# Kernel tuning notes

Hardware: AMD Instinct MI355X
Metric: run time of the kernel (lower is better)

The kernel has to match this reference:

```python
import jax, jax.numpy as jnp
import numpy as np


def setup_inputs() -> dict:
    key = jax.random.key(0)
    ks = jax.random.split(key, 10)
    B, N, F, H = 4, 512, 64, 4
    x = jax.random.normal(ks[0], (B, N, F), dtype=jnp.float32)
    adj = jax.random.uniform(ks[1], (N, N), dtype=jnp.float32)
    s = 1.0 / np.sqrt(F)
    Wq = jax.random.normal(ks[2], (F, F * H), dtype=jnp.float32) * s
    bq = jnp.zeros((F * H,), dtype=jnp.float32)
    Wk = jax.random.normal(ks[3], (F, F * H), dtype=jnp.float32) * s
    bk = jnp.zeros((F * H,), dtype=jnp.float32)
    Wlin = jax.random.normal(ks[4], (H, F), dtype=jnp.float32) * (1.0 / np.sqrt(H))
    blin = jnp.zeros((F,), dtype=jnp.float32)
    Wfc = jax.random.normal(ks[5], (F, F), dtype=jnp.float32) * s
    bfc = jnp.zeros((F,), dtype=jnp.float32)
    return {"x": x, "adj": adj, "Wq": Wq, "bq": bq, "Wk": Wk, "bk": bk,
            "Wlin": Wlin, "blin": blin, "Wfc": Wfc, "bfc": bfc}


def reference(x, adj, Wq, bq, Wk, bk, Wlin, blin, Wfc, bfc):
    B, N, F = x.shape
    H = Wlin.shape[0]
    # multi-head attention matrix (value projection is computed but unused in the original)
    q = (x @ Wq + bq).reshape(B, N, H, F)  # [B,N,H,F]
    k = (x @ Wk + bk).reshape(B, N, H, F)
    scores = jnp.einsum('bihf,bjhf->bhij', q, k) / jnp.sqrt(jnp.float32(F))
    attn = jax.nn.softmax(scores, axis=-1)  # [B,H,N,N]
    # linear over heads: [B,N,N,H] @ [H,F] -> [B,N,N,F]
    SV2 = jnp.einsum('bhij,hf->bijf', attn, Wlin) + blin
    # symmetric normalization of (adj + I)
    A = adj + jnp.eye(N, dtype=adj.dtype)
    d = jnp.sum(A, axis=1) ** -0.5
    noradj = d[:, None] * A * d[None, :]  # [N,N]
    # sum over dim 1 (source index i) of noradj[i,j]*SV2[b,i,j,f]*x[b,j,f]
    S = jnp.einsum('ij,bijf->bjf', noradj, SV2)
    sx = x * S  # [B,N,F]
    out = jnp.einsum('ij,bjf->bif', noradj, sx)
    out = out @ Wfc + bfc
    return jax.nn.relu(out)
```

## Files before the change

### kernel.cpp

```cpp
#include <hip/hip_runtime.h>
#include <math.h>

#define NN 512
#define FF 64
#define HH 4


__global__ __launch_bounds__(512) void k_s1(const float* __restrict__ x,
                                            const float* __restrict__ Wq,
                                            const float* __restrict__ bq,
                                            const float* __restrict__ Wk,
                                            const float* __restrict__ bk,
                                            const float* __restrict__ adj,
                                            float* __restrict__ q_t,
                                            float* __restrict__ kT,
                                            float* __restrict__ dinv,
                                            float* __restrict__ T,
                                            float* __restrict__ cvec) {
    __shared__ float x_lds[4][64];
    int blk = blockIdx.x, tid = threadIdx.x;
    int wave = tid >> 6, lane = tid & 63;
    int b = blk >> 7, itile = blk & 127;
    int i0 = itile * 4;

    if (wave >= 4) {
        int idx = tid - 256;
        x_lds[idx >> 6][idx & 63] = x[((long)b * NN + i0 + (idx >> 6)) * FF + (idx & 63)];
    } else if (wave == 0) {
        float acc = 0.f;
#pragma unroll
        for (int k = 0; k < 8; ++k) acc += adj[blk * NN + k * 64 + lane];
        for (int o = 32; o > 0; o >>= 1) acc += __shfl_xor(acc, o);
        if (lane == 0) dinv[blk] = 1.0f / sqrtf(acc + 1.0f);
    } else if (wave == 1) {
        if (lane < 16) T[blk * 16 + lane] = 0.f;
    } else if (wave == 2) {
        if (lane == 0) cvec[blk] = 0.f;
    }
    __syncthreads();

    int isK = tid >> 8, col = tid & 255;
    const float* W = isK ? Wk : Wq;
    float bv = (isK ? bk : bq)[col];
    float a0 = bv, a1 = bv, a2 = bv, a3 = bv;
#pragma unroll 8
    for (int cc = 0; cc < 64; ++cc) {
        float w = W[cc * 256 + col];
        a0 = fmaf(x_lds[0][cc], w, a0);
        a1 = fmaf(x_lds[1][cc], w, a1);
        a2 = fmaf(x_lds[2][cc], w, a2);
        a3 = fmaf(x_lds[3][cc], w, a3);
    }
    int h = col >> 6, f = col & 63;
    int bh = b * HH + h;
    if (!isK) {
        long base = ((long)bh * NN + i0) * FF + f;
        q_t[base] = a0; q_t[base + FF] = a1;
        q_t[base + 2 * FF] = a2; q_t[base + 3 * FF] = a3;
    } else {
        long base = ((long)bh * FF + f) * NN + i0;
        *(float4*)(kT + base) = make_float4(a0, a1, a2, a3);
    }
}

__global__ __launch_bounds__(512) void k_s2(const float* __restrict__ q_t,
                                            const float* __restrict__ kT,
                                            const float* __restrict__ adj,
                                            const float* __restrict__ dinv,
                                            float* __restrict__ T,
                                            float* __restrict__ cvec) {
    __shared__ float q_lds[8][64];
    __shared__ float red[8][8];
    __shared__ float red2[8][8];
    int blk = blockIdx.x, tid = threadIdx.x;
    int itile = blk & 63, h = (blk >> 6) & 3, b = blk >> 8;
    int bh = b * HH + h, i0 = itile * 8;
    int wv = tid >> 6, lane = tid & 63;

    q_lds[tid >> 6][tid & 63] = q_t[((long)bh * NN + i0 + (tid >> 6)) * FF + (tid & 63)];
    __syncthreads();

    int j = tid;
    const float* kb = kT + (long)bh * FF * NN;
    float s[8];
#pragma unroll
    for (int r = 0; r < 8; ++r) s[r] = 0.f;
#pragma unroll 2
    for (int f4 = 0; f4 < 64; f4 += 4) {
        float kv[4];
#pragma unroll
        for (int u = 0; u < 4; ++u) kv[u] = kb[(f4 + u) * NN + j];
#pragma unroll
        for (int r = 0; r < 8; ++r) {
            float4 qv = *(const float4*)&q_lds[r][f4];
            s[r] = fmaf(qv.x, kv[0], s[r]);
            s[r] = fmaf(qv.y, kv[1], s[r]);
            s[r] = fmaf(qv.z, kv[2], s[r]);
            s[r] = fmaf(qv.w, kv[3], s[r]);
        }
    }
    const float scale = 0.125f;
#pragma unroll
    for (int r = 0; r < 8; ++r) {
        float v = s[r];
        for (int o = 32; o > 0; o >>= 1) v = fmaxf(v, __shfl_xor(v, o));
        if (lane == 0) red[r][wv] = v;
    }
    __syncthreads();
    float m[8];
#pragma unroll
    for (int r = 0; r < 8; ++r) {
        float v = red[r][0];
#pragma unroll
        for (int w = 1; w < 8; ++w) v = fmaxf(v, red[r][w]);
        m[r] = v;
    }
#pragma unroll
    for (int r = 0; r < 8; ++r) {
        s[r] = expf((s[r] - m[r]) * scale);
        float v = s[r];
        for (int o = 32; o > 0; o >>= 1) v += __shfl_xor(v, o);
        if (lane == 0) red2[r][wv] = v;
    }
    __syncthreads();
    float Zi[8];
#pragma unroll
    for (int r = 0; r < 8; ++r) {
        float v = red2[r][0];
#pragma unroll
        for (int w = 1; w < 8; ++w) v += red2[r][w];
        Zi[r] = 1.0f / v;
    }
    float dj = dinv[j];
    float pw = 0.f, cw = 0.f;
#pragma unroll
    for (int r = 0; r < 8; ++r) {
        int gi = i0 + r;
        float di = dinv[gi];
        float a = adj[(long)gi * NN + j] + (gi == j ? 1.f : 0.f);
        float t = di * a;
        pw = fmaf(t, s[r] * Zi[r], pw);
        cw += t;
    }
    atomicAdd(&T[bh * NN + j], pw * dj);
    if (b == 0 && h == 0) atomicAdd(&cvec[j], cw);
}

__global__ __launch_bounds__(256) void k_s3(const float* __restrict__ x,
                                            const float* __restrict__ T,
                                            const float* __restrict__ Wlin,
                                            const float* __restrict__ blin,
                                            const float* __restrict__ cvec,
                                            const float* __restrict__ adj,
                                            const float* __restrict__ dinv,
                                            const float* __restrict__ Wfc,
                                            const float* __restrict__ bfc,
                                            float* __restrict__ out) {
    __shared__ float4 u4_l[NN];
    __shared__ float  u0_l[NN];
    __shared__ float2 ad_l[NN];
    __shared__ float part[4][2][64];
    __shared__ float m_lds[2][64];
    __shared__ float part2[4][2][64];
    int blk = blockIdx.x, tid = threadIdx.x;
    int b = blk >> 8, itile = blk & 255;
    int i0 = itile * 2;

    for (int jj = tid; jj < NN; jj += 256) {
        float dj = dinv[jj];
        u0_l[jj] = dj * dj * cvec[jj];
        u4_l[jj] = make_float4(dj * T[(b * HH + 0) * NN + jj],
                               dj * T[(b * HH + 1) * NN + jj],
                               dj * T[(b * HH + 2) * NN + jj],
                               dj * T[(b * HH + 3) * NN + jj]);
        ad_l[jj] = make_float2(adj[(long)i0 * NN + jj] + (i0 == jj ? 1.f : 0.f),
                               adj[(long)(i0 + 1) * NN + jj] + (i0 + 1 == jj ? 1.f : 0.f));
    }
    __syncthreads();

    int f = tid & 63, jc = tid >> 6;
    int jb = jc * 128;
    float blf = blin[f];
    float4 wl = make_float4(Wlin[f], Wlin[64 + f], Wlin[128 + f], Wlin[192 + f]);
    const float* xb = x + (long)b * NN * FF + f;
    float a0 = 0.f, a1 = 0.f;
#pragma unroll 4
    for (int j = jb; j < jb + 128; ++j) {
        float xv = xb[(long)j * FF];
        float4 u = u4_l[j];
        float2 ad = ad_l[j];
        float S = blf * u0_l[j];
        S = fmaf(wl.x, u.x, S);
        S = fmaf(wl.y, u.y, S);
        S = fmaf(wl.z, u.z, S);
        S = fmaf(wl.w, u.w, S);
        float sx = xv * S;
        a0 = fmaf(ad.x, sx, a0);
        a1 = fmaf(ad.y, sx, a1);
    }
    part[jc][0][f] = a0;
    part[jc][1][f] = a1;
    __syncthreads();
    if (jc == 0) {
        m_lds[0][f] = (part[0][0][f] + part[1][0][f] + part[2][0][f] + part[3][0][f]) * dinv[i0];
        m_lds[1][f] = (part[0][1][f] + part[1][1][f] + part[2][1][f] + part[3][1][f]) * dinv[i0 + 1];
    }
    __syncthreads();
    float o0 = 0.f, o1 = 0.f;
    int c0 = jc * 16;
#pragma unroll
    for (int cc = 0; cc < 16; ++cc) {
        float w = Wfc[(c0 + cc) * FF + f];
        o0 = fmaf(m_lds[0][c0 + cc], w, o0);
        o1 = fmaf(m_lds[1][c0 + cc], w, o1);
    }
    part2[jc][0][f] = o0;
    part2[jc][1][f] = o1;
    __syncthreads();
    if (jc == 0) {
        float bb = bfc[f];
        float r0 = part2[0][0][f] + part2[1][0][f] + part2[2][0][f] + part2[3][0][f] + bb;
        float r1 = part2[0][1][f] + part2[1][1][f] + part2[2][1][f] + part2[3][1][f] + bb;
        out[((long)b * NN + i0) * FF + f]     = fmaxf(r0, 0.f);
        out[((long)b * NN + i0 + 1) * FF + f] = fmaxf(r1, 0.f);
    }
}

extern "C" void kernel_launch(void* const* d_in, const int* in_sizes, int n_in,
                              void* d_out, int out_size, void* d_ws, size_t ws_size,
                              hipStream_t stream) {
    const float* x    = (const float*)d_in[0];
    const float* adj  = (const float*)d_in[1];
    const float* Wq   = (const float*)d_in[2];
    const float* bq   = (const float*)d_in[3];
    const float* Wk   = (const float*)d_in[4];
    const float* bk   = (const float*)d_in[5];
    const float* Wlin = (const float*)d_in[6];
    const float* blin = (const float*)d_in[7];
    const float* Wfc  = (const float*)d_in[8];
    const float* bfc  = (const float*)d_in[9];
    float* out = (float*)d_out;

    float* ws   = (float*)d_ws;
    float* dinv = ws;
    float* cvec = ws + 512;
    float* T    = ws + 1024;
    float* q_t  = ws + 9216;
    float* kT   = ws + 2106368;

    k_s1<<<dim3(512), dim3(512), 0, stream>>>(x, Wq, bq, Wk, bk, adj, q_t, kT, dinv, T, cvec);
    k_s2<<<dim3(1024), dim3(512), 0, stream>>>(q_t, kT, adj, dinv, T, cvec);
    k_s3<<<dim3(1024), dim3(256), 0, stream>>>(x, T, Wlin, blin, cvec, adj, dinv, Wfc, bfc, out);
}
```

Measured before the change: 117.2 us.

## Tile QK^T in LDS with register blocking and row-major K layout

The score kernel now handles 16 query rows per block and stages K in swizzled LDS tiles. Each thread computes a 2x8 register tile from float4 LDS reads, replacing the earlier per-column global reads of a transposed K. The projection kernel is split into separate Q and K blocks of 256 threads and writes K row-major. Partial sums are reduced with shuffles before the atomics, which cuts the atomic count. This aims to raise arithmetic reuse and coalescing in the attention stage, at the cost of more LDS traffic, extra barriers and higher register use.

```diff
diff --git a/kernel.cpp b/kernel.cpp
--- a/kernel.cpp
+++ b/kernel.cpp
@@ -6,144 +6,221 @@
 #define HH 4
 
 
-__global__ __launch_bounds__(512) void k_s1(const float* __restrict__ x,
+__global__ __launch_bounds__(256) void k_s1(const float* __restrict__ x,
                                             const float* __restrict__ Wq,
                                             const float* __restrict__ bq,
                                             const float* __restrict__ Wk,
                                             const float* __restrict__ bk,
                                             const float* __restrict__ adj,
                                             float* __restrict__ q_t,
-                                            float* __restrict__ kT,
+                                            float* __restrict__ k_t,
                                             float* __restrict__ dinv,
                                             float* __restrict__ T,
                                             float* __restrict__ cvec) {
     __shared__ float x_lds[4][64];
     int blk = blockIdx.x, tid = threadIdx.x;
     int wave = tid >> 6, lane = tid & 63;
-    int b = blk >> 7, itile = blk & 127;
-    int i0 = itile * 4;
-
-    if (wave >= 4) {
-        int idx = tid - 256;
-        x_lds[idx >> 6][idx & 63] = x[((long)b * NN + i0 + (idx >> 6)) * FF + (idx & 63)];
-    } else if (wave == 0) {
+
+    if (blk < 512 && wave == 0) {
         float acc = 0.f;
 #pragma unroll
-        for (int k = 0; k < 8; ++k) acc += adj[blk * NN + k * 64 + lane];
+        for (int k = 0; k < 8; ++k) acc += adj[(long)blk * NN + k * 64 + lane];
         for (int o = 32; o > 0; o >>= 1) acc += __shfl_xor(acc, o);
         if (lane == 0) dinv[blk] = 1.0f / sqrtf(acc + 1.0f);
-    } else if (wave == 1) {
-        if (lane < 16) T[blk * 16 + lane] = 0.f;
-    } else if (wave == 2) {
-        if (lane == 0) cvec[blk] = 0.f;
-    }
-    __syncthreads();
-
-    int isK = tid >> 8, col = tid & 255;
+    }
+    if (blk < 128 && wave == 1) T[blk * 64 + lane] = 0.f;
+    if (blk < 8 && wave == 2) cvec[blk * 64 + lane] = 0.f;
+
+    int b = blk >> 8, rest = blk & 255, isK = rest >> 7, itile = rest & 127;
+    int i0 = itile * 4;
+    x_lds[tid >> 6][tid & 63] = x[((long)b * NN + i0 + (tid >> 6)) * FF + (tid & 63)];
+    __syncthreads();
     const float* W = isK ? Wk : Wq;
-    float bv = (isK ? bk : bq)[col];
+    float bv = (isK ? bk : bq)[tid];
     float a0 = bv, a1 = bv, a2 = bv, a3 = bv;
-#pragma unroll 8
     for (int cc = 0; cc < 64; ++cc) {
-        float w = W[cc * 256 + col];
+        float w = W[cc * 256 + tid];
         a0 = fmaf(x_lds[0][cc], w, a0);
         a1 = fmaf(x_lds[1][cc], w, a1);
         a2 = fmaf(x_lds[2][cc], w, a2);
         a3 = fmaf(x_lds[3][cc], w, a3);
     }
-    int h = col >> 6, f = col & 63;
-    int bh = b * HH + h;
-    if (!isK) {
-        long base = ((long)bh * NN + i0) * FF + f;
-        q_t[base] = a0; q_t[base + FF] = a1;
-        q_t[base + 2 * FF] = a2; q_t[base + 3 * FF] = a3;
-    } else {
-        long base = ((long)bh * FF + f) * NN + i0;
-        *(float4*)(kT + base) = make_float4(a0, a1, a2, a3);
-    }
+    int h = tid >> 6, f = tid & 63;
+    float* dst = (isK ? k_t : q_t) + ((long)(b * HH + h) * NN + i0) * FF + f;
+    dst[0] = a0; dst[FF] = a1; dst[2 * FF] = a2; dst[3 * FF] = a3;
 }
 
 __global__ __launch_bounds__(512) void k_s2(const float* __restrict__ q_t,
-                                            const float* __restrict__ kT,
+                                            const float* __restrict__ k_t,
                                             const float* __restrict__ adj,
                                             const float* __restrict__ dinv,
                                             float* __restrict__ T,
                                             float* __restrict__ cvec) {
-    __shared__ float q_lds[8][64];
-    __shared__ float red[8][8];
-    __shared__ float red2[8][8];
+    __shared__ float ql[16 * 68];
+    __shared__ float kl[512 * 16];
+    __shared__ float redm[8][16];
+    __shared__ float redz[8][16];
     int blk = blockIdx.x, tid = threadIdx.x;
-    int itile = blk & 63, h = (blk >> 6) & 3, b = blk >> 8;
-    int bh = b * HH + h, i0 = itile * 8;
-    int wv = tid >> 6, lane = tid & 63;
-
-    q_lds[tid >> 6][tid & 63] = q_t[((long)bh * NN + i0 + (tid >> 6)) * FF + (tid & 63)];
-    __syncthreads();
-
-    int j = tid;
-    const float* kb = kT + (long)bh * FF * NN;
-    float s[8];
-#pragma unroll
-    for (int r = 0; r < 8; ++r) s[r] = 0.f;
-#pragma unroll 2
-    for (int f4 = 0; f4 < 64; f4 += 4) {
-        float kv[4];
-#pragma unroll
-        for (int u = 0; u < 4; ++u) kv[u] = kb[(f4 + u) * NN + j];
-#pragma unroll
-        for (int r = 0; r < 8; ++r) {
-            float4 qv = *(const float4*)&q_lds[r][f4];
-            s[r] = fmaf(qv.x, kv[0], s[r]);
-            s[r] = fmaf(qv.y, kv[1], s[r]);
-            s[r] = fmaf(qv.z, kv[2], s[r]);
-            s[r] = fmaf(qv.w, kv[3], s[r]);
-        }
-    }
+    int bh = blk >> 5, itile = blk & 31;
+    int i0 = itile * 16;
+    int wv = tid >> 6;
+    int ig = tid & 7, jg = tid >> 3;
+
+    if (tid < 256) {
+        int r = tid >> 4, c4 = tid & 15;
+        *(float4*)&ql[r * 68 + c4 * 4] =
+            *(const float4*)(q_t + ((long)bh * NN + i0 + r) * FF + c4 * 4);
+    }
+
+    float acc[2][8];
+#pragma unroll
+    for (int ii = 0; ii < 2; ++ii)
+#pragma unroll
+        for (int jj = 0; jj < 8; ++jj) acc[ii][jj] = 0.f;
+
+    const float* kb = k_t + (long)bh * NN * FF;
+#pragma unroll
+    for (int cc = 0; cc < 4; ++cc) {
+#pragma unroll
+        for (int w = 0; w < 4; ++w) {
+            int v = w * 512 + tid;
+            int row = v >> 2, c4 = v & 3;
+            int slot = c4 ^ ((row >> 3) & 3);
+            *(float4*)&kl[row * 16 + slot * 4] =
+                *(const float4*)(kb + (long)row * FF + cc * 16 + c4 * 4);
+        }
+        __syncthreads();
+#pragma unroll
+        for (int k4 = 0; k4 < 4; ++k4) {
+            float4 qf[2], kf[8];
+#pragma unroll
+            for (int ii = 0; ii < 2; ++ii)
+                qf[ii] = *(const float4*)&ql[(ig * 2 + ii) * 68 + cc * 16 + k4 * 4];
+#pragma unroll
+            for (int jj = 0; jj < 8; ++jj) {
+                int j = jg * 8 + jj;
+                int slot = k4 ^ ((j >> 3) & 3);
+                kf[jj] = *(const float4*)&kl[j * 16 + slot * 4];
+            }
+#pragma unroll
+            for (int ii = 0; ii < 2; ++ii)
+#pragma unroll
+                for (int jj = 0; jj < 8; ++jj) {
+                    acc[ii][jj] = fmaf(qf[ii].x, kf[jj].x, acc[ii][jj]);
+                    acc[ii][jj] = fmaf(qf[ii].y, kf[jj].y, acc[ii][jj]);
+                    acc[ii][jj] = fmaf(qf[ii].z, kf[jj].z, acc[ii][jj]);
+                    acc[ii][jj] = fmaf(qf[ii].w, kf[jj].w, acc[ii][jj]);
+                }
+        }
+        __syncthreads();
+    }
+
+#pragma unroll
+    for (int w = 0; w < 4; ++w) {
+        int v = w * 512 + tid;
+        int r = v >> 7, c4 = v & 127;
+        *(float4*)&kl[r * 512 + c4 * 4] =
+            *(const float4*)(adj + (long)(i0 + r) * NN + c4 * 4);
+    }
+
     const float scale = 0.125f;
-#pragma unroll
-    for (int r = 0; r < 8; ++r) {
-        float v = s[r];
-        for (int o = 32; o > 0; o >>= 1) v = fmaxf(v, __shfl_xor(v, o));
-        if (lane == 0) red[r][wv] = v;
-    }
-    __syncthreads();
-    float m[8];
-#pragma unroll
-    for (int r = 0; r < 8; ++r) {
-        float v = red[r][0];
-#pragma unroll
-        for (int w = 1; w < 8; ++w) v = fmaxf(v, red[r][w]);
-        m[r] = v;
-    }
-#pragma unroll
-    for (int r = 0; r < 8; ++r) {
-        s[r] = expf((s[r] - m[r]) * scale);
-        float v = s[r];
-        for (int o = 32; o > 0; o >>= 1) v += __shfl_xor(v, o);
-        if (lane == 0) red2[r][wv] = v;
-    }
-    __syncthreads();
-    float Zi[8];
-#pragma unroll
-    for (int r = 0; r < 8; ++r) {
-        float v = red2[r][0];
-#pragma unroll
-        for (int w = 1; w < 8; ++w) v += red2[r][w];
-        Zi[r] = 1.0f / v;
-    }
-    float dj = dinv[j];
-    float pw = 0.f, cw = 0.f;
-#pragma unroll
-    for (int r = 0; r < 8; ++r) {
-        int gi = i0 + r;
-        float di = dinv[gi];
-        float a = adj[(long)gi * NN + j] + (gi == j ? 1.f : 0.f);
-        float t = di * a;
-        pw = fmaf(t, s[r] * Zi[r], pw);
-        cw += t;
-    }
-    atomicAdd(&T[bh * NN + j], pw * dj);
-    if (b == 0 && h == 0) atomicAdd(&cvec[j], cw);
+    float m[2], Zi[2];
+#pragma unroll
+    for (int ii = 0; ii < 2; ++ii) {
+        float v = acc[ii][0];
+#pragma unroll
+        for (int jj = 1; jj < 8; ++jj) v = fmaxf(v, acc[ii][jj]);
+        v = fmaxf(v, __shfl_xor(v, 8));
+        v = fmaxf(v, __shfl_xor(v, 16));
+        v = fmaxf(v, __shfl_xor(v, 32));
+        if ((tid & 63) < 8) redm[wv][ig * 2 + ii] = v;
+    }
+    __syncthreads();
+#pragma unroll
+    for (int ii = 0; ii < 2; ++ii) {
+        int row = ig * 2 + ii;
+        float v = redm[0][row];
+#pragma unroll
+        for (int w = 1; w < 8; ++w) v = fmaxf(v, redm[w][row]);
+        m[ii] = v;
+    }
+#pragma unroll
+    for (int ii = 0; ii < 2; ++ii) {
+        float z = 0.f;
+#pragma unroll
+        for (int jj = 0; jj < 8; ++jj) {
+            float p = expf((acc[ii][jj] - m[ii]) * scale);
+            acc[ii][jj] = p;
+            z += p;
+        }
+        z += __shfl_xor(z, 8);
+        z += __shfl_xor(z, 16);
+        z += __shfl_xor(z, 32);
+        if ((tid & 63) < 8) redz[wv][ig * 2 + ii] = z;
+    }
+    __syncthreads();
+#pragma unroll
+    for (int ii = 0; ii < 2; ++ii) {
+        int row = ig * 2 + ii;
+        float z = redz[0][row];
+#pragma unroll
+        for (int w = 1; w < 8; ++w) z += redz[w][row];
+        Zi[ii] = 1.0f / z;
+    }
+
+    float di[2];
+    di[0] = dinv[i0 + ig * 2];
+    di[1] = dinv[i0 + ig * 2 + 1];
+    float cs[8], cw[8];
+#pragma unroll
+    for (int jj = 0; jj < 8; ++jj) { cs[jj] = 0.f; cw[jj] = 0.f; }
+#pragma unroll
+    for (int ii = 0; ii < 2; ++ii) {
+        int irow = ig * 2 + ii;
+        int gi = i0 + irow;
+        float av[8];
+        *(float4*)&av[0] = *(const float4*)&kl[irow * 512 + jg * 8];
+        *(float4*)&av[4] = *(const float4*)&kl[irow * 512 + jg * 8 + 4];
+        float dz = di[ii] * Zi[ii];
+#pragma unroll
+        for (int jj = 0; jj < 8; ++jj) {
+            int j = jg * 8 + jj;
+            float a = av[jj] + (gi == j ? 1.f : 0.f);
+            cs[jj] = fmaf(di[ii] * a * Zi[ii], acc[ii][jj], cs[jj]);
+            cw[jj] = fmaf(di[ii], a, cw[jj]);
+        }
+        (void)dz;
+    }
+#pragma unroll
+    for (int jj = 0; jj < 8; ++jj) {
+        float v = cs[jj];
+        v += __shfl_xor(v, 1);
+        v += __shfl_xor(v, 2);
+        v += __shfl_xor(v, 4);
+        cs[jj] = v;
+    }
+    if (bh == 0) {
+#pragma unroll
+        for (int jj = 0; jj < 8; ++jj) {
+            float w = cw[jj];
+            w += __shfl_xor(w, 1);
+            w += __shfl_xor(w, 2);
+            w += __shfl_xor(w, 4);
+            cw[jj] = w;
+        }
+    }
+    if (ig == 0) {
+#pragma unroll
+        for (int jj = 0; jj < 8; ++jj) {
+            int j = jg * 8 + jj;
+            atomicAdd(&T[bh * NN + j], cs[jj] * dinv[j]);
+        }
+        if (bh == 0) {
+#pragma unroll
+            for (int jj = 0; jj < 8; ++jj)
+                atomicAdd(&cvec[jg * 8 + jj], cw[jj]);
+        }
+    }
 }
 
 __global__ __launch_bounds__(256) void k_s3(const float* __restrict__ x,
@@ -246,9 +323,9 @@
     float* cvec = ws + 512;
     float* T    = ws + 1024;
     float* q_t  = ws + 9216;
-    float* kT   = ws + 2106368;
-
-    k_s1<<<dim3(512), dim3(512), 0, stream>>>(x, Wq, bq, Wk, bk, adj, q_t, kT, dinv, T, cvec);
-    k_s2<<<dim3(1024), dim3(512), 0, stream>>>(q_t, kT, adj, dinv, T, cvec);
+    float* k_t  = ws + 2106368;
+
+    k_s1<<<dim3(1024), dim3(256), 0, stream>>>(x, Wq, bq, Wk, bk, adj, q_t, k_t, dinv, T, cvec);
+    k_s2<<<dim3(512), dim3(512), 0, stream>>>(q_t, k_t, adj, dinv, T, cvec);
     k_s3<<<dim3(1024), dim3(256), 0, stream>>>(x, T, Wlin, blin, cvec, adj, dinv, Wfc, bfc, out);
 }
```

Result: slower. 120.9 us (+3.2%).

## Interleave K in float4 groups, split projection blocks finer, widen final kernel

Applied to the files above, without the earlier changes.

The K projection is now stored as groups of four features per key index, so the score kernel reads one float4 per key per step instead of four strided scalar loads. The projection kernel is split into 2048 smaller blocks that each handle two rows and either Q or K. Zero-initialisation of T and cvec moves to a subset of blocks. The final kernel uses 512 threads with half the j range per wave, and softmax switches to fast __expf. Finer blocks raise parallelism but add redundant loads of x and weights, and __expf gives slightly lower precision.

```diff
diff --git a/kernel.cpp b/kernel.cpp
--- a/kernel.cpp
+++ b/kernel.cpp
@@ -6,7 +6,7 @@
 #define HH 4
 
 
-__global__ __launch_bounds__(512) void k_s1(const float* __restrict__ x,
+__global__ __launch_bounds__(256) void k_s1(const float* __restrict__ x,
                                             const float* __restrict__ Wq,
                                             const float* __restrict__ bq,
                                             const float* __restrict__ Wk,
@@ -17,49 +17,41 @@
                                             float* __restrict__ dinv,
                                             float* __restrict__ T,
                                             float* __restrict__ cvec) {
-    __shared__ float x_lds[4][64];
+    __shared__ float x_lds[2][64];
     int blk = blockIdx.x, tid = threadIdx.x;
     int wave = tid >> 6, lane = tid & 63;
-    int b = blk >> 7, itile = blk & 127;
-    int i0 = itile * 4;
-
-    if (wave >= 4) {
-        int idx = tid - 256;
-        x_lds[idx >> 6][idx & 63] = x[((long)b * NN + i0 + (idx >> 6)) * FF + (idx & 63)];
-    } else if (wave == 0) {
+
+    if (blk < 512 && wave == 0) {
         float acc = 0.f;
 #pragma unroll
-        for (int k = 0; k < 8; ++k) acc += adj[blk * NN + k * 64 + lane];
+        for (int k = 0; k < 8; ++k) acc += adj[(long)blk * NN + k * 64 + lane];
         for (int o = 32; o > 0; o >>= 1) acc += __shfl_xor(acc, o);
         if (lane == 0) dinv[blk] = 1.0f / sqrtf(acc + 1.0f);
-    } else if (wave == 1) {
-        if (lane < 16) T[blk * 16 + lane] = 0.f;
-    } else if (wave == 2) {
-        if (lane == 0) cvec[blk] = 0.f;
-    }
-    __syncthreads();
-
-    int isK = tid >> 8, col = tid & 255;
+    }
+    if (blk < 128 && wave == 1) T[blk * 64 + lane] = 0.f;
+    if (blk < 8 && wave == 2) cvec[blk * 64 + lane] = 0.f;
+
+    int b = blk >> 9, rest = blk & 511, isK = rest >> 8, itile = rest & 255;
+    int i0 = itile * 2;
+    if (tid < 128)
+        x_lds[tid >> 6][tid & 63] = x[((long)b * NN + i0 + (tid >> 6)) * FF + (tid & 63)];
+    __syncthreads();
     const float* W = isK ? Wk : Wq;
-    float bv = (isK ? bk : bq)[col];
-    float a0 = bv, a1 = bv, a2 = bv, a3 = bv;
-#pragma unroll 8
+    float bv = (isK ? bk : bq)[tid];
+    float a0 = bv, a1 = bv;
     for (int cc = 0; cc < 64; ++cc) {
-        float w = W[cc * 256 + col];
+        float w = W[cc * 256 + tid];
         a0 = fmaf(x_lds[0][cc], w, a0);
         a1 = fmaf(x_lds[1][cc], w, a1);
-        a2 = fmaf(x_lds[2][cc], w, a2);
-        a3 = fmaf(x_lds[3][cc], w, a3);
-    }
-    int h = col >> 6, f = col & 63;
+    }
+    int h = tid >> 6, f = tid & 63;
     int bh = b * HH + h;
     if (!isK) {
         long base = ((long)bh * NN + i0) * FF + f;
         q_t[base] = a0; q_t[base + FF] = a1;
-        q_t[base + 2 * FF] = a2; q_t[base + 3 * FF] = a3;
     } else {
-        long base = ((long)bh * FF + f) * NN + i0;
-        *(float4*)(kT + base) = make_float4(a0, a1, a2, a3);
+        float* kp = kT + (((long)(bh * 16 + (f >> 2)) * NN + i0) << 2) + (f & 3);
+        kp[0] = a0; kp[4] = a1;
     }
 }
 
@@ -81,22 +73,20 @@
     __syncthreads();
 
     int j = tid;
-    const float* kb = kT + (long)bh * FF * NN;
+    const float4* kb4 = (const float4*)kT + (long)bh * 16 * NN;
     float s[8];
 #pragma unroll
     for (int r = 0; r < 8; ++r) s[r] = 0.f;
-#pragma unroll 2
-    for (int f4 = 0; f4 < 64; f4 += 4) {
-        float kv[4];
-#pragma unroll
-        for (int u = 0; u < 4; ++u) kv[u] = kb[(f4 + u) * NN + j];
+#pragma unroll 4
+    for (int g = 0; g < 16; ++g) {
+        float4 kv = kb4[g * NN + j];
 #pragma unroll
         for (int r = 0; r < 8; ++r) {
-            float4 qv = *(const float4*)&q_lds[r][f4];
-            s[r] = fmaf(qv.x, kv[0], s[r]);
-            s[r] = fmaf(qv.y, kv[1], s[r]);
-            s[r] = fmaf(qv.z, kv[2], s[r]);
-            s[r] = fmaf(qv.w, kv[3], s[r]);
+            float4 qv = *(const float4*)&q_lds[r][g * 4];
+            s[r] = fmaf(qv.x, kv.x, s[r]);
+            s[r] = fmaf(qv.y, kv.y, s[r]);
+            s[r] = fmaf(qv.z, kv.z, s[r]);
+            s[r] = fmaf(qv.w, kv.w, s[r]);
         }
     }
     const float scale = 0.125f;
@@ -117,7 +107,7 @@
     }
 #pragma unroll
     for (int r = 0; r < 8; ++r) {
-        s[r] = expf((s[r] - m[r]) * scale);
+        s[r] = __expf((s[r] - m[r]) * scale);
         float v = s[r];
         for (int o = 32; o > 0; o >>= 1) v += __shfl_xor(v, o);
         if (lane == 0) red2[r][wv] = v;
@@ -126,10 +116,10 @@
     float Zi[8];
 #pragma unroll
     for (int r = 0; r < 8; ++r) {
-        float v = red2[r][0];
-#pragma unroll
-        for (int w = 1; w < 8; ++w) v += red2[r][w];
-        Zi[r] = 1.0f / v;
+        float z = red2[r][0];
+#pragma unroll
+        for (int w = 1; w < 8; ++w) z += red2[r][w];
+        Zi[r] = 1.0f / z;
     }
     float dj = dinv[j];
     float pw = 0.f, cw = 0.f;
@@ -146,7 +136,7 @@
     if (b == 0 && h == 0) atomicAdd(&cvec[j], cw);
 }
 
-__global__ __launch_bounds__(256) void k_s3(const float* __restrict__ x,
+__global__ __launch_bounds__(512) void k_s3(const float* __restrict__ x,
                                             const float* __restrict__ T,
                                             const float* __restrict__ Wlin,
                                             const float* __restrict__ blin,
@@ -159,14 +149,15 @@
     __shared__ float4 u4_l[NN];
     __shared__ float  u0_l[NN];
     __shared__ float2 ad_l[NN];
-    __shared__ float part[4][2][64];
+    __shared__ float part[8][2][64];
     __shared__ float m_lds[2][64];
-    __shared__ float part2[4][2][64];
+    __shared__ float part2[8][2][64];
     int blk = blockIdx.x, tid = threadIdx.x;
     int b = blk >> 8, itile = blk & 255;
     int i0 = itile * 2;
 
-    for (int jj = tid; jj < NN; jj += 256) {
+    {
+        int jj = tid;
         float dj = dinv[jj];
         u0_l[jj] = dj * dj * cvec[jj];
         u4_l[jj] = make_float4(dj * T[(b * HH + 0) * NN + jj],
@@ -179,13 +170,13 @@
     __syncthreads();
 
     int f = tid & 63, jc = tid >> 6;
-    int jb = jc * 128;
+    int jb = jc * 64;
     float blf = blin[f];
     float4 wl = make_float4(Wlin[f], Wlin[64 + f], Wlin[128 + f], Wlin[192 + f]);
     const float* xb = x + (long)b * NN * FF + f;
     float a0 = 0.f, a1 = 0.f;
 #pragma unroll 4
-    for (int j = jb; j < jb + 128; ++j) {
+    for (int j = jb; j < jb + 64; ++j) {
         float xv = xb[(long)j * FF];
         float4 u = u4_l[j];
         float2 ad = ad_l[j];
@@ -202,14 +193,17 @@
     part[jc][1][f] = a1;
     __syncthreads();
     if (jc == 0) {
-        m_lds[0][f] = (part[0][0][f] + part[1][0][f] + part[2][0][f] + part[3][0][f]) * dinv[i0];
-        m_lds[1][f] = (part[0][1][f] + part[1][1][f] + part[2][1][f] + part[3][1][f]) * dinv[i0 + 1];
+        float s0 = 0.f, s1 = 0.f;
+#pragma unroll
+        for (int c = 0; c < 8; ++c) { s0 += part[c][0][f]; s1 += part[c][1][f]; }
+        m_lds[0][f] = s0 * dinv[i0];
+        m_lds[1][f] = s1 * dinv[i0 + 1];
     }
     __syncthreads();
     float o0 = 0.f, o1 = 0.f;
-    int c0 = jc * 16;
-#pragma unroll
-    for (int cc = 0; cc < 16; ++cc) {
+    int c0 = jc * 8;
+#pragma unroll
+    for (int cc = 0; cc < 8; ++cc) {
         float w = Wfc[(c0 + cc) * FF + f];
         o0 = fmaf(m_lds[0][c0 + cc], w, o0);
         o1 = fmaf(m_lds[1][c0 + cc], w, o1);
@@ -219,8 +213,9 @@
     __syncthreads();
     if (jc == 0) {
         float bb = bfc[f];
-        float r0 = part2[0][0][f] + part2[1][0][f] + part2[2][0][f] + part2[3][0][f] + bb;
-        float r1 = part2[0][1][f] + part2[1][1][f] + part2[2][1][f] + part2[3][1][f] + bb;
+        float r0 = bb, r1 = bb;
+#pragma unroll
+        for (int c = 0; c < 8; ++c) { r0 += part2[c][0][f]; r1 += part2[c][1][f]; }
         out[((long)b * NN + i0) * FF + f]     = fmaxf(r0, 0.f);
         out[((long)b * NN + i0 + 1) * FF + f] = fmaxf(r1, 0.f);
     }
@@ -248,7 +243,7 @@
     float* q_t  = ws + 9216;
     float* kT   = ws + 2106368;
 
-    k_s1<<<dim3(512), dim3(512), 0, stream>>>(x, Wq, bq, Wk, bk, adj, q_t, kT, dinv, T, cvec);
+    k_s1<<<dim3(2048), dim3(256), 0, stream>>>(x, Wq, bq, Wk, bk, adj, q_t, kT, dinv, T, cvec);
     k_s2<<<dim3(1024), dim3(512), 0, stream>>>(q_t, kT, adj, dinv, T, cvec);
-    k_s3<<<dim3(1024), dim3(256), 0, stream>>>(x, T, Wlin, blin, cvec, adj, dinv, Wfc, bfc, out);
-}
+    k_s3<<<dim3(1024), dim3(512), 0, stream>>>(x, T, Wlin, blin, cvec, adj, dinv, Wfc, bfc, out);
+}
```

Result: slower. 120.9 us (+3.2%).
